# Kernel tuning notes

Measured on AMD Instinct MI355X. Metric: run time of the kernel, lower is better.

The kernel has to match this reference:

```python
import jax, jax.numpy as jnp
import numpy as np

MARGIN_POS = 1.0
MARGIN_NEG = 0.2
LAMBDA_D = 250.0

B, D, H, W = 2, 128, 64, 64


def setup_inputs() -> dict:
    key = jax.random.key(0)
    k0, k1, k2 = jax.random.split(key, 3)
    descriptors_0 = jax.random.normal(k0, (B, D, H, W), dtype=jnp.float32)
    descriptors_1 = jax.random.normal(k1, (B, D, H, W), dtype=jnp.float32)
    similarity_mask = jax.random.randint(k2, (B, H, W, H, W), 0, 2).astype(jnp.bool_)
    return {
        "descriptors_0": descriptors_0,
        "descriptors_1": descriptors_1,
        "similarity_mask": similarity_mask,
    }


def reference(descriptors_0, descriptors_1, similarity_mask):
    # [B,D,H,W] x [B,D,H,W] -> [B,H,W,H,W] dense pairwise descriptor dot products
    dotprod = jnp.einsum('bdij,bdkl->bijkl', descriptors_0, descriptors_1)
    zero = jnp.zeros((), dtype=dotprod.dtype)
    pos_loss = jnp.maximum(zero, MARGIN_POS - dotprod) * LAMBDA_D
    neg_loss = jnp.maximum(zero, dotprod - MARGIN_NEG)
    return jnp.where(similarity_mask, pos_loss, neg_loss).mean()
```

## Files before the change

### kernel.cpp

```cpp
#include <hip/hip_runtime.h>
#include <stdint.h>

#define BN 2
#define DN 128
#define MN 4096
#define TOTAL_INV (1.0f / 33554432.0f)

typedef __attribute__((ext_vector_type(8))) short short8;
typedef __attribute__((ext_vector_type(4))) float f32x4;

__device__ static inline unsigned short f2bf(float x) {
  unsigned int u = __float_as_uint(x);
  u += 0x7fffu + ((u >> 16) & 1u);
  return (unsigned short)(u >> 16);
}

__device__ static inline void async16(const void* g, void* l) {
  __builtin_amdgcn_global_load_lds(
      (const __attribute__((address_space(1))) void*)g,
      (__attribute__((address_space(3))) void*)l, 16, 0, 0);
}

__global__ __launch_bounds__(256) void transpose_cvt(
    const float* __restrict__ s0, const float* __restrict__ s1,
    unsigned short* __restrict__ o0, unsigned short* __restrict__ o1) {
  __shared__ float tile[64][65];
  const int tx = threadIdx.x & 63;
  const int ty = threadIdx.x >> 6;
  const int m0 = blockIdx.x * 64;
  const int d0 = blockIdx.y * 64;
  const int b  = blockIdx.z & 1;
  const float* src = (blockIdx.z >> 1) ? s1 : s0;
  unsigned short* dst = (blockIdx.z >> 1) ? o1 : o0;
  src += (size_t)b * DN * MN;
  dst += (size_t)b * MN * DN;
#pragma unroll
  for (int i = 0; i < 16; ++i) {
    int dr = i * 4 + ty;
    tile[dr][tx] = src[(size_t)(d0 + dr) * MN + m0 + tx];
  }
  __syncthreads();
#pragma unroll
  for (int i = 0; i < 16; ++i) {
    int mr = i * 4 + ty;
    dst[(size_t)(m0 + mr) * DN + d0 + tx] = f2bf(tile[tx][mr]);
  }
}

__global__ __launch_bounds__(256) void gemm_loss(
    const unsigned short* __restrict__ A, const unsigned short* __restrict__ Bm,
    const void* __restrict__ maskp, float* __restrict__ out) {
  __shared__ __align__(16) unsigned short As[2][128 * 32];
  __shared__ __align__(16) unsigned short Bs[2][128 * 32];
  __shared__ __align__(16) unsigned char Ms[128 * 128];
  __shared__ float red[4];
  __shared__ int mask_is_u8;

  const int tid  = threadIdx.x;
  const int lane = tid & 63;
  const int wave = tid >> 6;
  const int wm = wave >> 1, wn = wave & 1;
  const int quad = lane >> 4;
  const int l16  = lane & 15;
  const int bn = blockIdx.x, bm = blockIdx.y, bz = blockIdx.z;

  if (tid == 0) mask_is_u8 = 0;
  __syncthreads();
  if (((const unsigned int*)maskp)[tid] & 0xFFFFFF00u) mask_is_u8 = 1;

  const unsigned short* Ab = A  + (size_t)bz * MN * DN + (size_t)(bm * 128) * DN;
  const unsigned short* Bb = Bm + (size_t)bz * MN * DN + (size_t)(bn * 128) * DN;

  f32x4 acc[4][4];
#pragma unroll
  for (int i = 0; i < 4; ++i)
#pragma unroll
    for (int j = 0; j < 4; ++j) acc[i][j] = (f32x4){0.f, 0.f, 0.f, 0.f};

  auto stage = [&](int sel, int kt) {
    const int k0 = kt * 32;
#pragma unroll
    for (int p = 0; p < 2; ++p) {
      int c = tid + p * 256;
      int row = c >> 2;
      int cq  = c & 3;
      async16(Ab + (size_t)row * DN + k0 + cq * 8, &As[sel][c * 8]);
      async16(Bb + (size_t)row * DN + k0 + cq * 8, &Bs[sel][c * 8]);
    }
  };
  auto compute = [&](int sel) {
    short8 af[4], bf[4];
#pragma unroll
    for (int mi = 0; mi < 4; ++mi)
      af[mi] = *(const short8*)(&As[sel][(wm * 64 + mi * 16 + l16) * 32 + quad * 8]);
#pragma unroll
    for (int ni = 0; ni < 4; ++ni)
      bf[ni] = *(const short8*)(&Bs[sel][(wn * 64 + ni * 16 + l16) * 32 + quad * 8]);
#pragma unroll
    for (int mi = 0; mi < 4; ++mi)
#pragma unroll
      for (int ni = 0; ni < 4; ++ni)
        acc[mi][ni] = __builtin_amdgcn_mfma_f32_16x16x32_bf16(
            af[mi], bf[ni], acc[mi][ni], 0, 0, 0);
  };

  stage(0, 0);
  __syncthreads();
  const int u8 = mask_is_u8;

  const unsigned char* mg = (const unsigned char*)maskp +
      ((size_t)bz * MN + (size_t)(bm * 128)) * MN + (size_t)(bn * 128);
  if (u8) {
#pragma unroll
    for (int p = 0; p < 4; ++p) {
      int c = tid + p * 256;
      int row = c >> 3, off = (c & 7) * 16;
      async16(mg + (size_t)row * MN + off, Ms + c * 16);
    }
  }
  stage(1, 1);
  compute(0);
  __syncthreads();
  stage(0, 2);
  compute(1);
  __syncthreads();
  stage(1, 3);
  compute(0);
  __syncthreads();
  compute(1);

  const size_t gbase =
      ((size_t)bz * MN + (size_t)(bm * 128 + wm * 64)) * MN + (size_t)(bn * 128 + wn * 64);
  const int* mi32 = (const int*)maskp;
  const int lrow0 = wm * 64, lcol0 = wn * 64;
  float lsum = 0.0f;
#pragma unroll
  for (int mi = 0; mi < 4; ++mi) {
#pragma unroll
    for (int ni = 0; ni < 4; ++ni) {
      f32x4 v = acc[mi][ni];
#pragma unroll
      for (int r = 0; r < 4; ++r) {
        int m = mi * 16 + quad * 4 + r;
        int n = ni * 16 + l16;
        int msk = u8 ? (int)Ms[(lrow0 + m) * 128 + lcol0 + n]
                     : mi32[gbase + (size_t)m * MN + n];
        float dot = v[r];
        float pos = fmaxf(0.0f, 1.0f - dot) * 250.0f;
        float neg = fmaxf(0.0f, dot - 0.2f);
        lsum += msk ? pos : neg;
      }
    }
  }
#pragma unroll
  for (int off = 32; off > 0; off >>= 1) lsum += __shfl_xor(lsum, off);
  if (lane == 0) red[wave] = lsum;
  __syncthreads();
  if (tid == 0) {
    float t = (red[0] + red[1] + red[2] + red[3]) * TOTAL_INV;
    atomicAdd(out, t);
  }
}

extern "C" void kernel_launch(void* const* d_in, const int* in_sizes, int n_in,
                              void* d_out, int out_size, void* d_ws, size_t ws_size,
                              hipStream_t stream) {
  const float* d0 = (const float*)d_in[0];
  const float* d1 = (const float*)d_in[1];
  const void* mask = d_in[2];
  float* out = (float*)d_out;

  unsigned short* Aw = (unsigned short*)d_ws;
  unsigned short* Bw = Aw + (size_t)BN * MN * DN;

  hipMemsetAsync(d_out, 0, sizeof(float), stream);

  dim3 g1(MN / 64, DN / 64, BN * 2), b1(256);
  transpose_cvt<<<g1, b1, 0, stream>>>(d0, d1, Aw, Bw);

  dim3 g2(MN / 128, MN / 128, BN), b2(256);
  gemm_loss<<<g2, b2, 0, stream>>>(Aw, Bw, mask, out);
}
```

Baseline: 210.3 us.

## Pre-tile mask and K-slab descriptors, replace atomic with partial-sum reduction

Result: no change. 213.8 us (+1.6%).

```diff
diff --git a/kernel.cpp b/kernel.cpp
--- a/kernel.cpp
+++ b/kernel.cpp
@@ -5,9 +5,14 @@
 #define DN 128
 #define MN 4096
 #define TOTAL_INV (1.0f / 33554432.0f)
+#define NTILE 32
+#define NBLK (NTILE * NTILE)
+#define PARTIALS (NBLK * BN)
+#define KSLAB ((size_t)MN * 32)
 
 typedef __attribute__((ext_vector_type(8))) short short8;
 typedef __attribute__((ext_vector_type(4))) float f32x4;
+typedef __attribute__((ext_vector_type(4))) unsigned int u32x4;
 
 __device__ static inline unsigned short f2bf(float x) {
   unsigned int u = __float_as_uint(x);
@@ -21,35 +26,78 @@
       (__attribute__((address_space(3))) void*)l, 16, 0, 0);
 }
 
-__global__ __launch_bounds__(256) void transpose_cvt(
+__global__ __launch_bounds__(256) void prep(
     const float* __restrict__ s0, const float* __restrict__ s1,
-    unsigned short* __restrict__ o0, unsigned short* __restrict__ o1) {
-  __shared__ float tile[64][65];
-  const int tx = threadIdx.x & 63;
-  const int ty = threadIdx.x >> 6;
-  const int m0 = blockIdx.x * 64;
-  const int d0 = blockIdx.y * 64;
-  const int b  = blockIdx.z & 1;
-  const float* src = (blockIdx.z >> 1) ? s1 : s0;
-  unsigned short* dst = (blockIdx.z >> 1) ? o1 : o0;
-  src += (size_t)b * DN * MN;
-  dst += (size_t)b * MN * DN;
-#pragma unroll
-  for (int i = 0; i < 16; ++i) {
-    int dr = i * 4 + ty;
-    tile[dr][tx] = src[(size_t)(d0 + dr) * MN + m0 + tx];
-  }
-  __syncthreads();
-#pragma unroll
-  for (int i = 0; i < 16; ++i) {
-    int mr = i * 4 + ty;
-    dst[(size_t)(m0 + mr) * DN + d0 + tx] = f2bf(tile[tx][mr]);
+    const void* __restrict__ maskp,
+    unsigned short* __restrict__ o0, unsigned short* __restrict__ o1,
+    unsigned char* __restrict__ tmask) {
+  __shared__ __align__(16) unsigned char sh[32 * 1040];
+  __shared__ int flag;
+  const int tid = threadIdx.x;
+  const int bid = blockIdx.x;
+
+  if (bid < 1024) {
+    if (tid == 0) flag = 0;
+    __syncthreads();
+    if (((const unsigned int*)maskp)[tid] & 0xFFFFFF00u) flag = 1;
+    __syncthreads();
+    if (!flag) return;
+
+    const int bz = bid >> 9;
+    const int m0 = (bid & 511) * 8;
+    const unsigned char* src =
+        (const unsigned char*)maskp + ((size_t)bz * MN + m0) * MN;
+#pragma unroll
+    for (int row = 0; row < 8; ++row) {
+      u32x4 v = *(const u32x4*)(src + (size_t)row * MN + tid * 16);
+      int c  = tid >> 3;
+      int nc = (tid & 7) * 16;
+      *(u32x4*)(sh + c * 1040 + row * 128 + nc) = v;
+    }
+    __syncthreads();
+    const int bm = m0 >> 7, r0 = m0 & 127;
+    unsigned char* ob =
+        tmask + ((size_t)(bz * NBLK + bm * NTILE)) * 16384 + r0 * 128;
+#pragma unroll
+    for (int it = 0; it < 8; ++it) {
+      int c = it * 4 + (tid >> 6);
+      int inner = (tid & 63) * 16;
+      u32x4 v = *(const u32x4*)(sh + c * 1040 + inner);
+      *(u32x4*)(ob + (size_t)c * 16384 + inner) = v;
+    }
+  } else {
+    float (*tile)[65] = (float(*)[65])sh;
+    const int t  = bid - 1024;
+    const int m0 = (t & 63) * 64;
+    const int d0 = ((t >> 6) & 1) * 64;
+    const int img = t >> 7;
+    const int b = img & 1;
+    const float* src = (img >> 1) ? s1 : s0;
+    unsigned short* dst = (img >> 1) ? o1 : o0;
+    src += (size_t)b * DN * MN;
+    dst += (size_t)b * 4 * KSLAB;
+    const int tx = tid & 63;
+    const int ty = tid >> 6;
+#pragma unroll
+    for (int i = 0; i < 16; ++i) {
+      int dr = i * 4 + ty;
+      tile[dr][tx] = src[(size_t)(d0 + dr) * MN + m0 + tx];
+    }
+    __syncthreads();
+    const int d = d0 + tx;
+    const size_t dbase = (size_t)(d >> 5) * MN * 32 + (d & 31);
+#pragma unroll
+    for (int i = 0; i < 16; ++i) {
+      int mr = i * 4 + ty;
+      dst[dbase + (size_t)(m0 + mr) * 32] = f2bf(tile[tx][mr]);
+    }
   }
 }
 
 __global__ __launch_bounds__(256) void gemm_loss(
     const unsigned short* __restrict__ A, const unsigned short* __restrict__ Bm,
-    const void* __restrict__ maskp, float* __restrict__ out) {
+    const void* __restrict__ maskp, const unsigned char* __restrict__ tmask,
+    float* __restrict__ partial) {
   __shared__ __align__(16) unsigned short As[2][128 * 32];
   __shared__ __align__(16) unsigned short Bs[2][128 * 32];
   __shared__ __align__(16) unsigned char Ms[128 * 128];
@@ -68,8 +116,8 @@
   __syncthreads();
   if (((const unsigned int*)maskp)[tid] & 0xFFFFFF00u) mask_is_u8 = 1;
 
-  const unsigned short* Ab = A  + (size_t)bz * MN * DN + (size_t)(bm * 128) * DN;
-  const unsigned short* Bb = Bm + (size_t)bz * MN * DN + (size_t)(bn * 128) * DN;
+  const unsigned short* Abase = A  + (size_t)bz * 4 * KSLAB + (size_t)(bm * 128) * 32;
+  const unsigned short* Bbase = Bm + (size_t)bz * 4 * KSLAB + (size_t)(bn * 128) * 32;
 
   f32x4 acc[4][4];
 #pragma unroll
@@ -78,14 +126,13 @@
     for (int j = 0; j < 4; ++j) acc[i][j] = (f32x4){0.f, 0.f, 0.f, 0.f};
 
   auto stage = [&](int sel, int kt) {
-    const int k0 = kt * 32;
+    const unsigned short* Ak = Abase + (size_t)kt * KSLAB;
+    const unsigned short* Bk = Bbase + (size_t)kt * KSLAB;
 #pragma unroll
     for (int p = 0; p < 2; ++p) {
       int c = tid + p * 256;
-      int row = c >> 2;
-      int cq  = c & 3;
-      async16(Ab + (size_t)row * DN + k0 + cq * 8, &As[sel][c * 8]);
-      async16(Bb + (size_t)row * DN + k0 + cq * 8, &Bs[sel][c * 8]);
+      async16(Ak + c * 8, &As[sel][c * 8]);
+      async16(Bk + c * 8, &Bs[sel][c * 8]);
     }
   };
   auto compute = [&](int sel) {
@@ -108,14 +155,13 @@
   __syncthreads();
   const int u8 = mask_is_u8;
 
-  const unsigned char* mg = (const unsigned char*)maskp +
-      ((size_t)bz * MN + (size_t)(bm * 128)) * MN + (size_t)(bn * 128);
   if (u8) {
+    const unsigned char* mt =
+        tmask + (size_t)(bz * NBLK + bm * NTILE + bn) * 16384;
 #pragma unroll
     for (int p = 0; p < 4; ++p) {
       int c = tid + p * 256;
-      int row = c >> 3, off = (c & 7) * 16;
-      async16(mg + (size_t)row * MN + off, Ms + c * 16);
+      async16(mt + c * 16, Ms + c * 16);
     }
   }
   stage(1, 1);
@@ -156,10 +202,21 @@
   for (int off = 32; off > 0; off >>= 1) lsum += __shfl_xor(lsum, off);
   if (lane == 0) red[wave] = lsum;
   __syncthreads();
-  if (tid == 0) {
-    float t = (red[0] + red[1] + red[2] + red[3]) * TOTAL_INV;
-    atomicAdd(out, t);
-  }
+  if (tid == 0)
+    partial[bz * NBLK + bm * NTILE + bn] = red[0] + red[1] + red[2] + red[3];
+}
+
+__global__ __launch_bounds__(256) void reduce_partials(
+    const float* __restrict__ p, float* __restrict__ out) {
+  __shared__ float red[4];
+  const int tid = threadIdx.x;
+  float s = 0.0f;
+  for (int i = tid; i < PARTIALS; i += 256) s += p[i];
+#pragma unroll
+  for (int off = 32; off > 0; off >>= 1) s += __shfl_xor(s, off);
+  if ((tid & 63) == 0) red[tid >> 6] = s;
+  __syncthreads();
+  if (tid == 0) out[0] = (red[0] + red[1] + red[2] + red[3]) * TOTAL_INV;
 }
 
 extern "C" void kernel_launch(void* const* d_in, const int* in_sizes, int n_in,
@@ -171,13 +228,15 @@
   float* out = (float*)d_out;
 
   unsigned short* Aw = (unsigned short*)d_ws;
-  unsigned short* Bw = Aw + (size_t)BN * MN * DN;
-
-  hipMemsetAsync(d_out, 0, sizeof(float), stream);
-
-  dim3 g1(MN / 64, DN / 64, BN * 2), b1(256);
-  transpose_cvt<<<g1, b1, 0, stream>>>(d0, d1, Aw, Bw);
-
-  dim3 g2(MN / 128, MN / 128, BN), b2(256);
-  gemm_loss<<<g2, b2, 0, stream>>>(Aw, Bw, mask, out);
-}
+  unsigned short* Bw = Aw + (size_t)BN * 4 * KSLAB;
+  unsigned char* tmask = (unsigned char*)d_ws + (4u << 20);
+  float* partial = (float*)((char*)d_ws + (40u << 20));
+
+  dim3 g1(1024 + 512), b1(256);
+  prep<<<g1, b1, 0, stream>>>(d0, d1, mask, Aw, Bw, tmask);
+
+  dim3 g2(NTILE, NTILE, BN), b2(256);
+  gemm_loss<<<g2, b2, 0, stream>>>(Aw, Bw, mask, tmask, partial);
+
+  reduce_partials<<<1, 256, 0, stream>>>(partial, out);
+}
```
